# Kernel tuning notes

Measured on AMD Instinct MI355X. Metric: run time of the kernel, lower is better.

The kernel has to match this reference:

```python
import jax, jax.numpy as jnp
import numpy as np

B, S, D = 64, 2048, 64  # (batch*heads, seq_len, head_dim)

def setup_inputs() -> dict:
    key = jax.random.key(0)
    kq, kk, kv = jax.random.split(key, 3)
    q = jax.random.normal(kq, (B, S, D), dtype=jnp.float32)
    k = jax.random.normal(kk, (B, S, D), dtype=jnp.float32)
    v = jax.random.normal(kv, (B, S, D), dtype=jnp.float32)
    return {"q": q, "k": k, "v": v}

def reference(q, k, v):
    # scores: [B, S, S] = q @ k^T (no scaling, matching the source module)
    scores = jnp.einsum('bqd,bkd->bqk', q, k)
    attn = jax.nn.softmax(scores, axis=-1)
    # dropout p=0.0 -> identity
    out = jnp.einsum('bqk,bkd->bqd', attn, v)
    return out
```

## Files before the change

### kernel.cpp

```cpp
#include <hip/hip_runtime.h>

typedef __attribute__((ext_vector_type(8))) __bf16 bf16x8;
typedef __attribute__((ext_vector_type(8))) _Float16 f16x8;
typedef __attribute__((ext_vector_type(4))) float f32x4;
typedef __attribute__((ext_vector_type(8))) unsigned short u16x8;

#define SDIM 2048
#define DDIM 64
#define NBATCH 64
#define LOG2E 1.44269504088896340736f

#if __has_builtin(__builtin_amdgcn_exp2f)
#define EXP2F __builtin_amdgcn_exp2f
#else
#define EXP2F exp2f
#endif

__device__ inline unsigned short f2bf(float f) {
  unsigned u = __builtin_bit_cast(unsigned, f);
  u += 0x7fffu + ((u >> 16) & 1u);
  return (unsigned short)(u >> 16);
}
__device__ inline unsigned short f2h(float f) {
  return __builtin_bit_cast(unsigned short, (_Float16)f);
}

__device__ inline void gload_lds16(const void* g, void* l) {
  __builtin_amdgcn_global_load_lds(
      (const __attribute__((address_space(1))) unsigned int*)g,
      (__attribute__((address_space(3))) unsigned int*)l, 16, 0, 0);
}

__device__ inline int rperm(int p) { return p ^ ((p >> 3) & 7); }

__global__ __launch_bounds__(256) void prep_kernel(
    const float* __restrict__ k, const float* __restrict__ v,
    unsigned short* __restrict__ khf, unsigned short* __restrict__ vtb) {
  __shared__ float tile[64][65];
  const int b = blockIdx.x >> 5;
  const int s0 = (blockIdx.x & 31) * 64;
  const size_t base = ((size_t)b * SDIM + s0) * DDIM;

  {
    const float* src = k + base + threadIdx.x * 16;
    f32x4 a = *(const f32x4*)src;
    f32x4 b4 = *(const f32x4*)(src + 4);
    f32x4 c4 = *(const f32x4*)(src + 8);
    f32x4 d4 = *(const f32x4*)(src + 12);
    u16x8 o0, o1;
#pragma unroll
    for (int j = 0; j < 4; ++j) {
      o0[j] = f2h(a[j] * LOG2E);
      o0[4 + j] = f2h(b4[j] * LOG2E);
      o1[j] = f2h(c4[j] * LOG2E);
      o1[4 + j] = f2h(d4[j] * LOG2E);
    }
    unsigned short* dst = khf + base + threadIdx.x * 16;
    *(u16x8*)dst = o0;
    *(u16x8*)(dst + 8) = o1;
  }

  {
    int row = threadIdx.x >> 2;
    int c16 = (threadIdx.x & 3) * 16;
    const float* src = v + base + (size_t)row * DDIM + c16;
#pragma unroll
    for (int c = 0; c < 4; ++c) {
      f32x4 f = *(const f32x4*)(src + 4 * c);
      tile[row][c16 + 4 * c + 0] = f[0];
      tile[row][c16 + 4 * c + 1] = f[1];
      tile[row][c16 + 4 * c + 2] = f[2];
      tile[row][c16 + 4 * c + 3] = f[3];
    }
    __syncthreads();
    int d = threadIdx.x >> 2;
    int sc = (threadIdx.x & 3) * 16;
    u16x8 a, c;
#pragma unroll
    for (int j = 0; j < 8; ++j) a[j] = f2bf(tile[sc + j][d]);
#pragma unroll
    for (int j = 0; j < 8; ++j) c[j] = f2bf(tile[sc + 8 + j][d]);
    unsigned short* dst = vtb + ((size_t)b * DDIM + d) * SDIM + s0 + sc;
    *(u16x8*)dst = a;
    *(u16x8*)(dst + 8) = c;
  }
}

__global__ __launch_bounds__(256) void attn_kernel(
    const float* __restrict__ q, const unsigned short* __restrict__ khf,
    const unsigned short* __restrict__ vt, float* __restrict__ out) {
  __shared__ __align__(16) unsigned short kf[8 * 512];
  __shared__ __align__(16) unsigned short vf[8 * 512];
  __shared__ __align__(16) unsigned short pf[16 * 512];

  const int bid = blockIdx.x;
  const int b = (bid & 7) * 8 + ((bid >> 3) >> 4);
  const int qt = (bid >> 3) & 15;
  const int tid = threadIdx.x;
  const int w = tid >> 6;
  const int L = tid & 63;
  const int l15 = L & 15;
  const int l4 = L >> 4;

  const size_t boff = (size_t)b * (SDIM * DDIM);
  const int qg = qt * 128 + w * 32;

  f16x8 qa[2][2];
#pragma unroll
  for (int t = 0; t < 2; ++t)
#pragma unroll
    for (int c = 0; c < 2; ++c) {
      const float* src = q + boff + (size_t)(qg + t * 16 + l15) * DDIM + c * 32 + l4 * 8;
      f32x4 f0 = *(const f32x4*)(src);
      f32x4 f1 = *(const f32x4*)(src + 4);
      f16x8 h;
#pragma unroll
      for (int j = 0; j < 4; ++j) {
        h[j] = (_Float16)f0[j];
        h[4 + j] = (_Float16)f1[j];
      }
      qa[t][c] = h;
    }

  u16x8 uo;
#pragma unroll
  for (int j = 0; j < 8; ++j) uo[j] = 0x3F80;
  const bf16x8 ones = __builtin_bit_cast(bf16x8, uo);

  int pw[2][4];
#pragma unroll
  for (int n1 = 0; n1 < 2; ++n1)
#pragma unroll
    for (int r = 0; r < 4; ++r) {
      int lane2 = l4 * 4 + r + (n1 * 2 + (l15 >> 3)) * 16;
      pw[n1][r] = rperm(lane2) * 8 + (L & 7);
    }
  const int prd = rperm(L) * 8;

  f32x4 o[2][4], lacc[2];
#pragma unroll
  for (int t = 0; t < 2; ++t) {
#pragma unroll
    for (int n = 0; n < 4; ++n) o[t][n] = (f32x4){0.f, 0.f, 0.f, 0.f};
    lacc[t] = (f32x4){0.f, 0.f, 0.f, 0.f};
  }

  for (int kt = 0; kt < SDIM; kt += 64) {
    __syncthreads();
#pragma unroll
    for (int ff = 0; ff < 4; ++ff) {
      int f = w * 4 + ff;
      if (f < 8) {
        int n = f >> 1, c = f & 1;
        gload_lds16(khf + boff + (size_t)(kt + n * 16 + l15) * DDIM + c * 32 + l4 * 8,
                    &kf[f * 512]);
      } else {
        int fg = f - 8, n = fg >> 1, c = fg & 1;
        gload_lds16(vt + boff + (size_t)(n * 16 + l15) * SDIM + kt + c * 32 + l4 * 8,
                    &vf[fg * 512]);
      }
    }
    __syncthreads();

#pragma unroll
    for (int n = 0; n < 4; ++n) {
      f16x8 k0 = *(const f16x8*)&kf[(n * 2 + 0) * 512 + L * 8];
      f16x8 k1 = *(const f16x8*)&kf[(n * 2 + 1) * 512 + L * 8];
#pragma unroll
      for (int t = 0; t < 2; ++t) {
        f32x4 acc = (f32x4){0.f, 0.f, 0.f, 0.f};
        acc = __builtin_amdgcn_mfma_f32_16x16x32_f16(qa[t][0], k0, acc, 0, 0, 0);
        acc = __builtin_amdgcn_mfma_f32_16x16x32_f16(qa[t][1], k1, acc, 0, 0, 0);
        int fp = (w * 4 + t * 2 + (n >> 1)) * 512;
#pragma unroll
        for (int r = 0; r < 4; ++r) {
          float p = EXP2F(acc[r]);
          unsigned u = __builtin_bit_cast(unsigned, p);
          pf[fp + pw[n & 1][r]] = (unsigned short)((u + 0x8000u) >> 16);
        }
      }
    }

#pragma unroll
    for (int t = 0; t < 2; ++t) {
      bf16x8 p0 = *(const bf16x8*)&pf[(w * 4 + t * 2 + 0) * 512 + prd];
      bf16x8 p1 = *(const bf16x8*)&pf[(w * 4 + t * 2 + 1) * 512 + prd];
      lacc[t] = __builtin_amdgcn_mfma_f32_16x16x32_bf16(p0, ones, lacc[t], 0, 0, 0);
      lacc[t] = __builtin_amdgcn_mfma_f32_16x16x32_bf16(p1, ones, lacc[t], 0, 0, 0);
#pragma unroll
      for (int n = 0; n < 4; ++n) {
        bf16x8 v0 = *(const bf16x8*)&vf[(n * 2 + 0) * 512 + L * 8];
        bf16x8 v1 = *(const bf16x8*)&vf[(n * 2 + 1) * 512 + L * 8];
        o[t][n] = __builtin_amdgcn_mfma_f32_16x16x32_bf16(p0, v0, o[t][n], 0, 0, 0);
        o[t][n] = __builtin_amdgcn_mfma_f32_16x16x32_bf16(p1, v1, o[t][n], 0, 0, 0);
      }
    }
  }

#pragma unroll
  for (int t = 0; t < 2; ++t) {
    float rc[4];
#pragma unroll
    for (int r = 0; r < 4; ++r) rc[r] = 1.f / lacc[t][r];
#pragma unroll
    for (int n = 0; n < 4; ++n)
#pragma unroll
      for (int r = 0; r < 4; ++r)
        out[boff + (size_t)(qg + t * 16 + l4 * 4 + r) * DDIM + n * 16 + l15] =
            o[t][n][r] * rc[r];
  }
}

extern "C" void kernel_launch(void* const* d_in, const int* in_sizes, int n_in,
                              void* d_out, int out_size, void* d_ws, size_t ws_size,
                              hipStream_t stream) {
  const float* q = (const float*)d_in[0];
  const float* k = (const float*)d_in[1];
  const float* v = (const float*)d_in[2];
  float* out = (float*)d_out;
  unsigned short* khf = (unsigned short*)d_ws;
  unsigned short* vt = khf + (size_t)NBATCH * SDIM * DDIM;

  prep_kernel<<<NBATCH * (SDIM / 64), 256, 0, stream>>>(k, v, khf, vt);
  attn_kernel<<<NBATCH * (SDIM / 128), 256, 0, stream>>>(q, khf, vt, out);
}
```

Baseline: 241.3 us.

## Double-buffer K/V tiles in LDS and double per-block query tile size

The attention kernel now prefetches the next K/V tile into a second LDS buffer while computing on the current one, which removes one barrier per iteration and hides global-load latency. Each block now handles 256 query rows (64 per wave) instead of 128, so every K/V tile loaded is reused twice as much and fewer blocks are launched. Per-wave P scratch is preallocated and launch bounds request 2 blocks per CU. In exchange, register pressure rises (more accumulators and Q fragments) and the grid halves to 512 blocks, which reduces available parallelism.

```diff
diff --git a/kernel.cpp b/kernel.cpp
--- a/kernel.cpp
+++ b/kernel.cpp
@@ -86,16 +86,15 @@
   }
 }
 
-__global__ __launch_bounds__(256) void attn_kernel(
+__global__ __launch_bounds__(256, 2) void attn_kernel(
     const float* __restrict__ q, const unsigned short* __restrict__ khf,
     const unsigned short* __restrict__ vt, float* __restrict__ out) {
-  __shared__ __align__(16) unsigned short kf[8 * 512];
-  __shared__ __align__(16) unsigned short vf[8 * 512];
-  __shared__ __align__(16) unsigned short pf[16 * 512];
+  __shared__ __align__(16) unsigned short kv[2 * 16 * 512];
+  __shared__ __align__(16) unsigned short pf[4 * 8 * 512];
 
   const int bid = blockIdx.x;
-  const int b = (bid & 7) * 8 + ((bid >> 3) >> 4);
-  const int qt = (bid >> 3) & 15;
+  const int b = (bid & 7) * 8 + (bid >> 6);
+  const int qt = (bid >> 3) & 7;
   const int tid = threadIdx.x;
   const int w = tid >> 6;
   const int L = tid & 63;
@@ -103,11 +102,11 @@
   const int l4 = L >> 4;
 
   const size_t boff = (size_t)b * (SDIM * DDIM);
-  const int qg = qt * 128 + w * 32;
-
-  f16x8 qa[2][2];
-#pragma unroll
-  for (int t = 0; t < 2; ++t)
+  const int qg = qt * 256 + w * 64;
+
+  f16x8 qa[4][2];
+#pragma unroll
+  for (int t = 0; t < 4; ++t)
 #pragma unroll
     for (int c = 0; c < 2; ++c) {
       const float* src = q + boff + (size_t)(qg + t * 16 + l15) * DDIM + c * 32 + l4 * 8;
@@ -136,61 +135,81 @@
       pw[n1][r] = rperm(lane2) * 8 + (L & 7);
     }
   const int prd = rperm(L) * 8;
-
-  f32x4 o[2][4], lacc[2];
-#pragma unroll
-  for (int t = 0; t < 2; ++t) {
+  unsigned short* pwave = pf + w * 4096;
+
+  const unsigned short* gsrc[4];
+  int gadv;
+  if (w < 2) {
+#pragma unroll
+    for (int ff = 0; ff < 4; ++ff) {
+      int f = w * 4 + ff;
+      gsrc[ff] = khf + boff + (size_t)((f >> 1) * 16 + l15) * DDIM + (f & 1) * 32 + l4 * 8;
+    }
+    gadv = 64 * DDIM;
+  } else {
+#pragma unroll
+    for (int ff = 0; ff < 4; ++ff) {
+      int fg = (w - 2) * 4 + ff;
+      gsrc[ff] = vt + boff + (size_t)((fg >> 1) * 16 + l15) * SDIM + (fg & 1) * 32 + l4 * 8;
+    }
+    gadv = 64;
+  }
+  const int fdbase = w * 4;
+
+  f32x4 o[4][4], lacc[4];
+#pragma unroll
+  for (int t = 0; t < 4; ++t) {
 #pragma unroll
     for (int n = 0; n < 4; ++n) o[t][n] = (f32x4){0.f, 0.f, 0.f, 0.f};
     lacc[t] = (f32x4){0.f, 0.f, 0.f, 0.f};
   }
 
-  for (int kt = 0; kt < SDIM; kt += 64) {
+#pragma unroll
+  for (int ff = 0; ff < 4; ++ff) gload_lds16(gsrc[ff], &kv[(fdbase + ff) * 512]);
+#pragma unroll
+  for (int ff = 0; ff < 4; ++ff) gsrc[ff] += gadv;
+
+  for (int it = 0; it < SDIM / 64; ++it) {
+    const int cur = it & 1;
     __syncthreads();
-#pragma unroll
-    for (int ff = 0; ff < 4; ++ff) {
-      int f = w * 4 + ff;
-      if (f < 8) {
-        int n = f >> 1, c = f & 1;
-        gload_lds16(khf + boff + (size_t)(kt + n * 16 + l15) * DDIM + c * 32 + l4 * 8,
-                    &kf[f * 512]);
-      } else {
-        int fg = f - 8, n = fg >> 1, c = fg & 1;
-        gload_lds16(vt + boff + (size_t)(n * 16 + l15) * SDIM + kt + c * 32 + l4 * 8,
-                    &vf[fg * 512]);
-      }
-    }
-    __syncthreads();
+    if (it + 1 < SDIM / 64) {
+#pragma unroll
+      for (int ff = 0; ff < 4; ++ff)
+        gload_lds16(gsrc[ff], &kv[(1 - cur) * 8192 + (fdbase + ff) * 512]);
+#pragma unroll
+      for (int ff = 0; ff < 4; ++ff) gsrc[ff] += gadv;
+    }
+    const unsigned short* kvc = &kv[cur * 8192];
 
 #pragma unroll
     for (int n = 0; n < 4; ++n) {
-      f16x8 k0 = *(const f16x8*)&kf[(n * 2 + 0) * 512 + L * 8];
-      f16x8 k1 = *(const f16x8*)&kf[(n * 2 + 1) * 512 + L * 8];
-#pragma unroll
-      for (int t = 0; t < 2; ++t) {
+      f16x8 k0 = *(const f16x8*)&kvc[(n * 2 + 0) * 512 + L * 8];
+      f16x8 k1 = *(const f16x8*)&kvc[(n * 2 + 1) * 512 + L * 8];
+#pragma unroll
+      for (int t = 0; t < 4; ++t) {
         f32x4 acc = (f32x4){0.f, 0.f, 0.f, 0.f};
         acc = __builtin_amdgcn_mfma_f32_16x16x32_f16(qa[t][0], k0, acc, 0, 0, 0);
         acc = __builtin_amdgcn_mfma_f32_16x16x32_f16(qa[t][1], k1, acc, 0, 0, 0);
-        int fp = (w * 4 + t * 2 + (n >> 1)) * 512;
+        int fp = (t * 2 + (n >> 1)) * 512;
 #pragma unroll
         for (int r = 0; r < 4; ++r) {
           float p = EXP2F(acc[r]);
           unsigned u = __builtin_bit_cast(unsigned, p);
-          pf[fp + pw[n & 1][r]] = (unsigned short)((u + 0x8000u) >> 16);
+          pwave[fp + pw[n & 1][r]] = (unsigned short)((u + 0x8000u) >> 16);
         }
       }
     }
 
 #pragma unroll
-    for (int t = 0; t < 2; ++t) {
-      bf16x8 p0 = *(const bf16x8*)&pf[(w * 4 + t * 2 + 0) * 512 + prd];
-      bf16x8 p1 = *(const bf16x8*)&pf[(w * 4 + t * 2 + 1) * 512 + prd];
+    for (int t = 0; t < 4; ++t) {
+      bf16x8 p0 = *(const bf16x8*)&pwave[(t * 2 + 0) * 512 + prd];
+      bf16x8 p1 = *(const bf16x8*)&pwave[(t * 2 + 1) * 512 + prd];
       lacc[t] = __builtin_amdgcn_mfma_f32_16x16x32_bf16(p0, ones, lacc[t], 0, 0, 0);
       lacc[t] = __builtin_amdgcn_mfma_f32_16x16x32_bf16(p1, ones, lacc[t], 0, 0, 0);
 #pragma unroll
       for (int n = 0; n < 4; ++n) {
-        bf16x8 v0 = *(const bf16x8*)&vf[(n * 2 + 0) * 512 + L * 8];
-        bf16x8 v1 = *(const bf16x8*)&vf[(n * 2 + 1) * 512 + L * 8];
+        bf16x8 v0 = *(const bf16x8*)&kvc[(8 + n * 2 + 0) * 512 + L * 8];
+        bf16x8 v1 = *(const bf16x8*)&kvc[(8 + n * 2 + 1) * 512 + L * 8];
         o[t][n] = __builtin_amdgcn_mfma_f32_16x16x32_bf16(p0, v0, o[t][n], 0, 0, 0);
         o[t][n] = __builtin_amdgcn_mfma_f32_16x16x32_bf16(p1, v1, o[t][n], 0, 0, 0);
       }
@@ -198,7 +217,7 @@
   }
 
 #pragma unroll
-  for (int t = 0; t < 2; ++t) {
+  for (int t = 0; t < 4; ++t) {
     float rc[4];
 #pragma unroll
     for (int r = 0; r < 4; ++r) rc[r] = 1.f / lacc[t][r];
@@ -222,5 +241,5 @@
   unsigned short* vt = khf + (size_t)NBATCH * SDIM * DDIM;
 
   prep_kernel<<<NBATCH * (SDIM / 64), 256, 0, stream>>>(k, v, khf, vt);
-  attn_kernel<<<NBATCH * (SDIM / 128), 256, 0, stream>>>(q, khf, vt, out);
-}
+  attn_kernel<<<NBATCH * (SDIM / 256), 256, 0, stream>>>(q, khf, vt, out);
+}
```

New measurement: 225.4 us. -6.6%, faster.
